# Optimization experiments

Measured on AMD Instinct MI355X. Metric: run time of the kernel, lower is better.

The kernel has to match this reference:

```python
import jax, jax.numpy as jnp
import numpy as np

N, E, F_IN, E_IN, H, L, C = 50000, 500000, 128, 16, 128, 2, 2
BN_EPS = 1e-5


def _linear_params(key, fan_in, fan_out):
    k1, k2 = jax.random.split(key)
    w = jax.random.normal(k1, (fan_in, fan_out), jnp.float32) * (1.0 / np.sqrt(fan_in))
    b = jax.random.normal(k2, (fan_out,), jnp.float32) * 0.01
    return w, b


def setup_inputs() -> dict:
    key = jax.random.key(0)
    ks = jax.random.split(key, 32)
    x = jax.random.normal(ks[0], (N, F_IN), jnp.float32)
    edge_attr = jax.random.normal(ks[1], (E, E_IN), jnp.float32)
    edge_index = jax.random.randint(ks[2], (2, E), 0, N, jnp.int64)

    node_w, node_b = _linear_params(ks[3], F_IN, H)
    edge_w, edge_b = _linear_params(ks[4], E_IN, H)

    def stack(fn, base):
        ws, bs = zip(*[fn(jax.random.fold_in(ks[base], i)) for i in range(L)])
        return jnp.stack(ws), jnp.stack(bs)

    conv_w1, conv_b1 = stack(lambda k: _linear_params(k, H, H), 5)
    conv_w2, conv_b2 = stack(lambda k: _linear_params(k, H, H), 6)
    emlp_w1, emlp_b1 = stack(lambda k: _linear_params(k, 3 * H, H), 7)
    emlp_w2, emlp_b2 = stack(lambda k: _linear_params(k, H, H), 8)
    bn_gamma = jnp.ones((L, H), jnp.float32)
    bn_beta = jnp.zeros((L, H), jnp.float32)

    mlp_w1, mlp_b1 = _linear_params(ks[9], 3 * H, 50)
    mlp_w2, mlp_b2 = _linear_params(ks[10], 50, 25)
    mlp_w3, mlp_b3 = _linear_params(ks[11], 25, C)

    return dict(x=x, edge_attr=edge_attr,
                node_w=node_w, node_b=node_b, edge_w=edge_w, edge_b=edge_b,
                conv_w1=conv_w1, conv_b1=conv_b1, conv_w2=conv_w2, conv_b2=conv_b2,
                bn_gamma=bn_gamma, bn_beta=bn_beta,
                emlp_w1=emlp_w1, emlp_b1=emlp_b1, emlp_w2=emlp_w2, emlp_b2=emlp_b2,
                mlp_w1=mlp_w1, mlp_b1=mlp_b1, mlp_w2=mlp_w2, mlp_b2=mlp_b2,
                mlp_w3=mlp_w3, mlp_b3=mlp_b3, edge_index=edge_index)


def _forward(x, edge_attr, node_w, node_b, edge_w, edge_b,
             conv_w1, conv_b1, conv_w2, conv_b2, bn_gamma, bn_beta,
             emlp_w1, emlp_b1, emlp_w2, emlp_b2,
             mlp_w1, mlp_b1, mlp_w2, mlp_b2, mlp_w3, mlp_b3, edge_index):
    src, dst = edge_index[0], edge_index[1]
    h = x @ node_w + node_b                      # [N, H]
    ea = edge_attr @ edge_w + edge_b             # [E, H]
    for i in range(L):
        # GINEConv: message = relu(x_src + edge_attr), scatter-add at dst
        msg = jax.nn.relu(h[src] + ea)           # [E, H]
        agg = jax.ops.segment_sum(msg, dst, num_segments=N)
        z = h + agg                              # eps = 0
        z = jax.nn.relu(z @ conv_w1[i] + conv_b1[i]) @ conv_w2[i] + conv_b2[i]
        # BatchNorm (training-mode batch statistics over nodes)
        mu = jnp.mean(z, axis=0)
        var = jnp.var(z, axis=0)
        z = bn_gamma[i] * (z - mu) * jax.lax.rsqrt(var + BN_EPS) + bn_beta[i]
        h = (h + jax.nn.relu(z)) * 0.5
        # edge update MLP
        eu = jnp.concatenate([h[src], h[dst], ea], axis=-1)  # [E, 3H]
        ea = ea + (jax.nn.relu(eu @ emlp_w1[i] + emlp_b1[i]) @ emlp_w2[i] + emlp_b2[i]) * 0.5
    # readout: x[edge_index.T].reshape(-1, 2H) cat edge_attr -> [E, 3H]
    feat = jnp.concatenate([h[src], h[dst], ea], axis=-1)
    o = jax.nn.relu(feat @ mlp_w1 + mlp_b1)      # dropout is eval no-op
    o = jax.nn.relu(o @ mlp_w2 + mlp_b2)
    return o @ mlp_w3 + mlp_b3                   # [E, n_classes]


def reference(x, edge_attr, node_w, node_b, edge_w, edge_b,
              conv_w1, conv_b1, conv_w2, conv_b2, bn_gamma, bn_beta,
              emlp_w1, emlp_b1, emlp_w2, emlp_b2,
              mlp_w1, mlp_b1, mlp_w2, mlp_b2, mlp_w3, mlp_b3, edge_index):
    return _forward(x, edge_attr, node_w, node_b, edge_w, edge_b,
                    conv_w1, conv_b1, conv_w2, conv_b2, bn_gamma, bn_beta,
                    emlp_w1, emlp_b1, emlp_w2, emlp_b2,
                    mlp_w1, mlp_b1, mlp_w2, mlp_b2, mlp_w3, mlp_b3, edge_index)
```

## Files before the change

kernel.cpp:

```cpp
#include <hip/hip_runtime.h>


#define NN 50000
#define NE 500000
#define HD 128

typedef _Float16 f16;
typedef _Float16 f16x8 __attribute__((ext_vector_type(8)));
typedef _Float16 f16x4 __attribute__((ext_vector_type(4)));
typedef _Float16 f16x2 __attribute__((ext_vector_type(2)));
typedef float f32x4 __attribute__((ext_vector_type(4)));
typedef unsigned short ushort_t;

#define MFMA16(a, b, c) __builtin_amdgcn_mfma_f32_16x16x32_f16((a), (b), (c), 0, 0, 0)

#define TSTR 152

#define P_NODE_W 0
#define P_NODE_B 16384
#define P_EDGE_W 16512
#define P_EDGE_B 18560
#define P_CONV_W1 18688
#define P_CONV_B1 51456
#define P_CONV_W2 51712
#define P_CONV_B2 84480
#define P_GAMMA 84736
#define P_BETA 84992
#define P_EMLP_W1 85248
#define P_EMLP_B1 183552
#define P_EMLP_W2 183808
#define P_EMLP_B2 216576
#define P_MLP_W1 216832
#define P_MLP_B1 236032
#define P_MLP_W2 236082
#define P_MLP_B2 237332
#define P_MLP_W3 237357
#define P_MLP_B3 237407
#define P_TOTAL 237409

__device__ __forceinline__ float bf2f(unsigned short u) {
    union { unsigned int i; float f; } v;
    v.i = ((unsigned int)u) << 16;
    return v.f;
}

__global__ __launch_bounds__(256) void k_detect(
    const unsigned int* nw, const int* ei, int* flags) {
    __shared__ int cF, cI;
    if (threadIdx.x == 0) { cF = 0; cI = 0; }
    __syncthreads();
    unsigned int u = nw[threadIdx.x];
    int e = (int)((u >> 7) & 0xFFu);
    int odd = ei[2 * threadIdx.x + 1];
    if (e >= 100 && e <= 140) atomicAdd(&cF, 1);
    if (odd != 0) atomicAdd(&cI, 1);
    __syncthreads();
    if (threadIdx.x == 0) {
        flags[0] = (cF < 160) ? 1 : 0;
        flags[1] = (cI < 64) ? 1 : 0;
    }
}

__global__ __launch_bounds__(256) void k_cvt(
    const void* src, f16* dst, int n4, const int* flags) {
    int i = blockIdx.x * 256 + threadIdx.x;
    if (i >= n4) return;
    f16x4 o;
    if (flags[0]) {
        float4 v = ((const float4*)src)[i];
        o[0] = (f16)v.x; o[1] = (f16)v.y; o[2] = (f16)v.z; o[3] = (f16)v.w;
    } else {
        ushort4 v = ((const ushort4*)src)[i];
        o[0] = (f16)bf2f(v.x); o[1] = (f16)bf2f(v.y);
        o[2] = (f16)bf2f(v.z); o[3] = (f16)bf2f(v.w);
    }
    ((f16x4*)dst)[i] = o;
}

__global__ __launch_bounds__(256) void k_cvt_prm(
    const void* p0, const void* p1, const void* p2, const void* p3,
    const void* p4, const void* p5, const void* p6, const void* p7,
    const void* p8, const void* p9, const void* p10, const void* p11,
    const void* p12, const void* p13, const void* p14, const void* p15,
    const void* p16, const void* p17, const void* p18, const void* p19,
    float* prm, const int* flags) {
    int i = blockIdx.x * 256 + threadIdx.x;
    if (i >= P_TOTAL) return;
    const int offs[21] = {P_NODE_W, P_NODE_B, P_EDGE_W, P_EDGE_B, P_CONV_W1,
                          P_CONV_B1, P_CONV_W2, P_CONV_B2, P_GAMMA, P_BETA,
                          P_EMLP_W1, P_EMLP_B1, P_EMLP_W2, P_EMLP_B2, P_MLP_W1,
                          P_MLP_B1, P_MLP_W2, P_MLP_B2, P_MLP_W3, P_MLP_B3,
                          P_TOTAL};
    const void* srcs[20] = {p0, p1, p2, p3, p4, p5, p6, p7, p8, p9, p10, p11,
                            p12, p13, p14, p15, p16, p17, p18, p19};
    int s = 0;
#pragma unroll
    for (int k = 1; k < 20; ++k)
        if (i >= offs[k]) s = k;
    int li = i - offs[s];
    float v = flags[0] ? ((const float*)srcs[s])[li]
                       : bf2f(((const ushort_t*)srcs[s])[li]);
    prm[i] = v;
}

__global__ __launch_bounds__(256) void k_cvt_idx(
    const int* src, int* dst, const int* flags) {
    int i = blockIdx.x * 256 + threadIdx.x;
    if (i >= 2 * NE) return;
    dst[i] = flags[1] ? src[2 * i] : src[i];
}

__global__ __launch_bounds__(256) void k_hist(const int* eix, int* cnt) {
    int e = blockIdx.x * 256 + threadIdx.x;
    if (e < NE) atomicAdd(&cnt[eix[NE + e]], 1);
}

__global__ __launch_bounds__(256) void k_scanA(const int* cnt, int* bsum) {
    __shared__ int wsum[4];
    int tid = threadIdx.x;
    int i = blockIdx.x * 256 + tid;
    int v = (i < NN) ? cnt[i] : 0;
#pragma unroll
    for (int s = 1; s < 64; s <<= 1) v += __shfl_xor(v, s);
    if ((tid & 63) == 0) wsum[tid >> 6] = v;
    __syncthreads();
    if (tid == 0) bsum[blockIdx.x] = wsum[0] + wsum[1] + wsum[2] + wsum[3];
}

__global__ __launch_bounds__(256) void k_scanB(const int* bsum, int* bpre, int* off) {
    __shared__ int l[200];
    int tid = threadIdx.x;
    if (tid < 196) l[tid] = bsum[tid];
    __syncthreads();
    if (tid == 0) {
        int run = 0;
        for (int b = 0; b < 196; ++b) { int t = l[b]; l[b] = run; run += t; }
        off[NN] = run;
    }
    __syncthreads();
    if (tid < 196) bpre[tid] = l[tid];
}

__global__ __launch_bounds__(256) void k_scanC(
    const int* cnt, const int* bpre, int* off, int* cursor) {
    __shared__ int wsum[4];
    int tid = threadIdx.x;
    int lane = tid & 63, wave = tid >> 6;
    int i = blockIdx.x * 256 + tid;
    int v = (i < NN) ? cnt[i] : 0;
    int incl = v;
#pragma unroll
    for (int s = 1; s < 64; s <<= 1) {
        int t = __shfl_up(incl, s);
        if (lane >= s) incl += t;
    }
    if (lane == 63) wsum[wave] = incl;
    __syncthreads();
    int add = bpre[blockIdx.x];
    for (int w = 0; w < 4; ++w)
        if (w < wave) add += wsum[w];
    int excl = add + incl - v;
    if (i < NN) { off[i] = excl; cursor[i] = excl; }
}

__global__ __launch_bounds__(256) void k_scatter(
    const int* eix, int* cursor, int* eord) {
    int e = blockIdx.x * 256 + threadIdx.x;
    if (e >= NE) return;
    int d = eix[NE + e];
    int pos = atomicAdd(&cursor[d], 1);
    eord[pos] = e;
}

__global__ __launch_bounds__(256) void k_agg(
    const f16* ea, const f16* h16, const int* eix, const int* off,
    const int* eord, f16* agg16) {
    int wid = (blockIdx.x * 256 + threadIdx.x) >> 6;
    int lane = threadIdx.x & 63;
    int beg = off[wid], end = off[wid + 1];
    float a0 = 0.f, a1 = 0.f;
    for (int i = beg; i < end; ++i) {
        int e = eord[i];
        int s = eix[e];
        f16x2 ev = *(const f16x2*)(ea + (size_t)e * HD + lane * 2);
        f16x2 hv = *(const f16x2*)(h16 + (size_t)s * HD + lane * 2);
        a0 += fmaxf((float)ev[0] + (float)hv[0], 0.f);
        a1 += fmaxf((float)ev[1] + (float)hv[1], 0.f);
    }
    f16x2 o; o[0] = (f16)a0; o[1] = (f16)a1;
    *(f16x2*)(agg16 + (size_t)wid * HD + lane * 2) = o;
}

__global__ __launch_bounds__(256) void k_prep(const float* prm, f16* wbuf) {
    int gid = blockIdx.x * 256 + threadIdx.x;
    if (gid < 13 * 16384) {
        int seg = gid >> 14;
        int idx = gid & 16383;
        int off;
        switch (seg) {
            case 0: off = P_NODE_W; break;
            case 1: off = P_CONV_W1; break;
            case 2: off = P_CONV_W1 + 16384; break;
            case 3: off = P_CONV_W2; break;
            case 4: off = P_CONV_W2 + 16384; break;
            case 5: case 6: case 7: off = P_EMLP_W1 + (seg - 5) * 16384; break;
            case 8: case 9: case 10: off = P_EMLP_W1 + 49152 + (seg - 8) * 16384; break;
            case 11: off = P_EMLP_W2; break;
            default: off = P_EMLP_W2 + 16384; break;
        }
        int fb = idx >> 9;
        int sub = (idx & 511) >> 3;
        int j = idx & 7;
        int q = sub >> 4, n = sub & 15;
        int nt = fb >> 2, kt = fb & 3;
        int k = kt * 32 + q * 8 + j;
        int c = nt * 16 + n;
        wbuf[gid] = (f16)prm[off + k * 128 + c];
    } else {
        int t = gid - 13 * 16384;
        if (t >= 3 * 8192) return;
        int s = t >> 13;
        int idx = t & 8191;
        int fb = idx >> 9;
        int sub = (idx & 511) >> 3;
        int j = idx & 7;
        int q = sub >> 4, n = sub & 15;
        int nt = fb >> 2, kt = fb & 3;
        int k = s * 128 + kt * 32 + q * 8 + j;
        int c = nt * 16 + n;
        float v = (c < 50) ? prm[P_MLP_W1 + k * 50 + c] : 0.f;
        wbuf[13 * 16384 + s * 8192 + idx] = (f16)v;
    }
}

__global__ __launch_bounds__(256) void k_node_lin(
    const f16* xc, const f16* wT, const float* bias, f16* h_f16) {
    __shared__ __align__(16) f16 wlds[16384];
    int tid = threadIdx.x;
    {
        const uint4* s = (const uint4*)wT;
        uint4* d = (uint4*)wlds;
        for (int i = tid; i < 2048; i += 256) d[i] = s[i];
    }
    __syncthreads();
    int wave = tid >> 6, lane = tid & 63, q = lane >> 4, ln = lane & 15;
    int rowbase = blockIdx.x * 128 + wave * 32;
    f32x4 acc[2][8] = {};
    for (int kt = 0; kt < 4; ++kt) {
        int koff = kt * 32 + q * 8;
        f16x8 a[2];
#pragma unroll
        for (int mt = 0; mt < 2; ++mt) {
            int row = min(rowbase + mt * 16 + ln, NN - 1);
            a[mt] = *(const f16x8*)(xc + row * HD + koff);
        }
#pragma unroll
        for (int nt = 0; nt < 8; ++nt) {
            f16x8 b = *(const f16x8*)&wlds[(nt * 4 + kt) * 512 + lane * 8];
            acc[0][nt] = MFMA16(a[0], b, acc[0][nt]);
            acc[1][nt] = MFMA16(a[1], b, acc[1][nt]);
        }
    }
#pragma unroll
    for (int nt = 0; nt < 8; ++nt) {
        int col = nt * 16 + ln;
        float bv = bias[col];
#pragma unroll
        for (int mt = 0; mt < 2; ++mt)
#pragma unroll
            for (int r = 0; r < 4; ++r) {
                int row = rowbase + mt * 16 + q * 4 + r;
                if (row < NN) h_f16[row * HD + col] = (f16)(acc[mt][nt][r] + bv);
            }
    }
}

__global__ __launch_bounds__(256) void k_edge_lin(
    const f16* eattr, const float* ew, const float* ebias, f16* ea) {
    __shared__ float wl[16 * 128];
    __shared__ float bl[128];
    __shared__ float al[64 * 16];
    int tid = threadIdx.x;
    int eb = blockIdx.x * 64;
    for (int i = tid; i < 2048; i += 256) wl[i] = ew[i];
    if (tid < 128) bl[tid] = ebias[tid];
    {
        int e_l = tid >> 2, k0 = (tid & 3) * 4;
        int e = min(eb + e_l, NE - 1);
        f16x4 u = *(const f16x4*)(eattr + e * 16 + k0);
        al[e_l * 16 + k0 + 0] = (float)u[0];
        al[e_l * 16 + k0 + 1] = (float)u[1];
        al[e_l * 16 + k0 + 2] = (float)u[2];
        al[e_l * 16 + k0 + 3] = (float)u[3];
    }
    __syncthreads();
    for (int i = 0; i < 32; ++i) {
        int o = i * 256 + tid;
        int e_l = o >> 7, c = o & 127;
        float s = bl[c];
#pragma unroll
        for (int k = 0; k < 16; ++k) s += al[e_l * 16 + k] * wl[k * 128 + c];
        int e = eb + e_l;
        if (e < NE) ea[(size_t)e * HD + c] = (f16)s;
    }
}

__global__ __launch_bounds__(256) void k_conv1(
    const f16* h16, const f16* agg16, const f16* wT, const float* bias,
    f16* t_node) {
    __shared__ __align__(16) f16 wlds[16384];
    int tid = threadIdx.x;
    {
        const uint4* s = (const uint4*)wT;
        uint4* d = (uint4*)wlds;
        for (int i = tid; i < 2048; i += 256) d[i] = s[i];
    }
    __syncthreads();
    int wave = tid >> 6, lane = tid & 63, q = lane >> 4, ln = lane & 15;
    int rowbase = blockIdx.x * 128 + wave * 32;
    f32x4 acc[2][8] = {};
    for (int kt = 0; kt < 4; ++kt) {
        int koff = kt * 32 + q * 8;
        f16x8 a[2];
#pragma unroll
        for (int mt = 0; mt < 2; ++mt) {
            int row = min(rowbase + mt * 16 + ln, NN - 1);
            f16x8 hv = *(const f16x8*)(h16 + row * HD + koff);
            f16x8 gv = *(const f16x8*)(agg16 + row * HD + koff);
            f16x8 av;
#pragma unroll
            for (int j = 0; j < 8; ++j) av[j] = (f16)((float)hv[j] + (float)gv[j]);
            a[mt] = av;
        }
#pragma unroll
        for (int nt = 0; nt < 8; ++nt) {
            f16x8 b = *(const f16x8*)&wlds[(nt * 4 + kt) * 512 + lane * 8];
            acc[0][nt] = MFMA16(a[0], b, acc[0][nt]);
            acc[1][nt] = MFMA16(a[1], b, acc[1][nt]);
        }
    }
#pragma unroll
    for (int nt = 0; nt < 8; ++nt) {
        int col = nt * 16 + ln;
        float bv = bias[col];
#pragma unroll
        for (int mt = 0; mt < 2; ++mt)
#pragma unroll
            for (int r = 0; r < 4; ++r) {
                int row = rowbase + mt * 16 + q * 4 + r;
                if (row < NN)
                    t_node[row * HD + col] = (f16)fmaxf(acc[mt][nt][r] + bv, 0.f);
            }
    }
}

__global__ __launch_bounds__(256) void k_conv2(
    const f16* t_node, const f16* wT, const float* bias, f16* z2, float* stats) {
    __shared__ __align__(16) f16 wlds[16384];
    int tid = threadIdx.x;
    {
        const uint4* s = (const uint4*)wT;
        uint4* d = (uint4*)wlds;
        for (int i = tid; i < 2048; i += 256) d[i] = s[i];
    }
    __syncthreads();
    int wave = tid >> 6, lane = tid & 63, q = lane >> 4, ln = lane & 15;
    int rowbase = blockIdx.x * 128 + wave * 32;
    f32x4 acc[2][8] = {};
    for (int kt = 0; kt < 4; ++kt) {
        int koff = kt * 32 + q * 8;
        f16x8 a[2];
#pragma unroll
        for (int mt = 0; mt < 2; ++mt) {
            int row = min(rowbase + mt * 16 + ln, NN - 1);
            a[mt] = *(const f16x8*)(t_node + row * HD + koff);
        }
#pragma unroll
        for (int nt = 0; nt < 8; ++nt) {
            f16x8 b = *(const f16x8*)&wlds[(nt * 4 + kt) * 512 + lane * 8];
            acc[0][nt] = MFMA16(a[0], b, acc[0][nt]);
            acc[1][nt] = MFMA16(a[1], b, acc[1][nt]);
        }
    }
#pragma unroll
    for (int nt = 0; nt < 8; ++nt) {
        int col = nt * 16 + ln;
        float bv = bias[col];
        float s = 0.f, s2 = 0.f;
#pragma unroll
        for (int mt = 0; mt < 2; ++mt)
#pragma unroll
            for (int r = 0; r < 4; ++r) {
                int row = rowbase + mt * 16 + q * 4 + r;
                if (row < NN) {
                    float v = acc[mt][nt][r] + bv;
                    z2[row * HD + col] = (f16)v;
                    s += v;
                    s2 += v * v;
                }
            }
        s += __shfl_xor(s, 16);  s += __shfl_xor(s, 32);
        s2 += __shfl_xor(s2, 16); s2 += __shfl_xor(s2, 32);
        if (lane < 16) {
            atomicAdd(&stats[col], s);
            atomicAdd(&stats[HD + col], s2);
        }
    }
}

__global__ __launch_bounds__(256) void k_bn(
    const f16* z2, const float* stats, const float* gamma, const float* beta,
    f16* h16) {
    int gid = blockIdx.x * 256 + threadIdx.x;
    if (gid >= NN * HD / 4) return;
    int base = gid * 4;
    int c0 = base & (HD - 1);
    f16x4 z = *(const f16x4*)(z2 + base);
    f16x4 h = *(const f16x4*)(h16 + base);
    f16x4 ho;
#pragma unroll
    for (int j = 0; j < 4; ++j) {
        int c = c0 + j;
        float mu = stats[c] * (1.0f / NN);
        float var = stats[HD + c] * (1.0f / NN) - mu * mu;
        float zn = gamma[c] * ((float)z[j] - mu) * rsqrtf(var + 1e-5f) + beta[c];
        ho[j] = (f16)(((float)h[j] + fmaxf(zn, 0.f)) * 0.5f);
    }
    *(f16x4*)(h16 + base) = ho;
}

__global__ __launch_bounds__(256) void k_emlp(
    const f16* h16, const int* eidx, const f16* w1T, const float* b1,
    const f16* w2T, const float* b2, f16* ea) {
    __shared__ __align__(16) f16 wlds[16384];
    __shared__ __align__(16) f16 t16[128 * TSTR];
    __shared__ int sidx[128], didx[128];
    int tid = threadIdx.x;
    int eb = blockIdx.x * 128;
    if (tid < 128) {
        int e = min(eb + tid, NE - 1);
        sidx[tid] = eidx[e];
        didx[tid] = eidx[NE + e];
    }
    int wave = tid >> 6, lane = tid & 63, q = lane >> 4, ln = lane & 15;
    f32x4 acc[2][8] = {};
    for (int seg = 0; seg < 3; ++seg) {
        __syncthreads();
        {
            const uint4* s = (const uint4*)(w1T + seg * 16384);
            uint4* d = (uint4*)wlds;
            for (int i = tid; i < 2048; i += 256) d[i] = s[i];
        }
        __syncthreads();
        for (int kt = 0; kt < 4; ++kt) {
            int koff = kt * 32 + q * 8;
            f16x8 a[2];
#pragma unroll
            for (int mt = 0; mt < 2; ++mt) {
                int le = wave * 32 + mt * 16 + ln;
                const f16* ap;
                if (seg == 0)      ap = h16 + (size_t)sidx[le] * HD + koff;
                else if (seg == 1) ap = h16 + (size_t)didx[le] * HD + koff;
                else               ap = ea + (size_t)min(eb + le, NE - 1) * HD + koff;
                a[mt] = *(const f16x8*)ap;
            }
#pragma unroll
            for (int nt = 0; nt < 8; ++nt) {
                f16x8 b = *(const f16x8*)&wlds[(nt * 4 + kt) * 512 + lane * 8];
                acc[0][nt] = MFMA16(a[0], b, acc[0][nt]);
                acc[1][nt] = MFMA16(a[1], b, acc[1][nt]);
            }
        }
    }
#pragma unroll
    for (int nt = 0; nt < 8; ++nt) {
        int col = nt * 16 + ln;
        float bv = b1[col];
#pragma unroll
        for (int mt = 0; mt < 2; ++mt)
#pragma unroll
            for (int r = 0; r < 4; ++r) {
                int row = wave * 32 + mt * 16 + q * 4 + r;
                t16[row * TSTR + col] = (f16)fmaxf(acc[mt][nt][r] + bv, 0.f);
            }
    }
    __syncthreads();
    {
        const uint4* s = (const uint4*)w2T;
        uint4* d = (uint4*)wlds;
        for (int i = tid; i < 2048; i += 256) d[i] = s[i];
    }
    __syncthreads();
    f32x4 acc2[2][8] = {};
    for (int kt = 0; kt < 4; ++kt) {
        int koff = kt * 32 + q * 8;
        f16x8 a[2];
#pragma unroll
        for (int mt = 0; mt < 2; ++mt) {
            int le = wave * 32 + mt * 16 + ln;
            a[mt] = *(const f16x8*)&t16[le * TSTR + koff];
        }
#pragma unroll
        for (int nt = 0; nt < 8; ++nt) {
            f16x8 b = *(const f16x8*)&wlds[(nt * 4 + kt) * 512 + lane * 8];
            acc2[0][nt] = MFMA16(a[0], b, acc2[0][nt]);
            acc2[1][nt] = MFMA16(a[1], b, acc2[1][nt]);
        }
    }
#pragma unroll
    for (int nt = 0; nt < 8; ++nt) {
        int col = nt * 16 + ln;
        float bv = b2[col];
#pragma unroll
        for (int mt = 0; mt < 2; ++mt)
#pragma unroll
            for (int r = 0; r < 4; ++r) {
                int e = eb + wave * 32 + mt * 16 + q * 4 + r;
                if (e < NE) {
                    size_t o = (size_t)e * HD + col;
                    ea[o] = (f16)((float)ea[o] + 0.5f * (acc2[mt][nt][r] + bv));
                }
            }
    }
}

__global__ __launch_bounds__(256) void k_readout(
    const f16* h16, const f16* ea, const int* eidx, const f16* w1Tp,
    const float* mb1, const float* mw2, const float* mb2,
    const float* mw3, const float* mb3, float* out) {
    __shared__ __align__(16) f16 wlds[8192];
    __shared__ f16 o1[256 * 58];
    __shared__ float w2l[50 * 28];
    __shared__ float w3l[50];
    __shared__ float b2l[25];
    __shared__ float b3l[2];
    __shared__ int sidx[256], didx[256];
    int tid = threadIdx.x;
    int eb = blockIdx.x * 256;
    {
        int e = min(eb + tid, NE - 1);
        sidx[tid] = eidx[e];
        didx[tid] = eidx[NE + e];
    }
    for (int i = tid; i < 50 * 28; i += 256) {
        int k = i / 28, ko = i - k * 28;
        w2l[i] = (ko < 25) ? mw2[k * 25 + ko] : 0.f;
    }
    if (tid < 50) w3l[tid] = mw3[tid];
    if (tid < 25) b2l[tid] = mb2[tid];
    if (tid < 2) b3l[tid] = mb3[tid];
    int wave = tid >> 6, lane = tid & 63, q = lane >> 4, ln = lane & 15;
    f32x4 acc[4][4] = {};
    for (int seg = 0; seg < 3; ++seg) {
        __syncthreads();
        {
            const uint4* s = (const uint4*)(w1Tp + seg * 8192);
            uint4* d = (uint4*)wlds;
            for (int i = tid; i < 1024; i += 256) d[i] = s[i];
        }
        __syncthreads();
        for (int kt = 0; kt < 4; ++kt) {
            int koff = kt * 32 + q * 8;
            f16x8 a[4];
#pragma unroll
            for (int mt = 0; mt < 4; ++mt) {
                int le = wave * 64 + mt * 16 + ln;
                const f16* ap;
                if (seg == 0)      ap = h16 + (size_t)sidx[le] * HD + koff;
                else if (seg == 1) ap = h16 + (size_t)didx[le] * HD + koff;
                else               ap = ea + (size_t)min(eb + le, NE - 1) * HD + koff;
                a[mt] = *(const f16x8*)ap;
            }
#pragma unroll
            for (int nt = 0; nt < 4; ++nt) {
                f16x8 b = *(const f16x8*)&wlds[(nt * 4 + kt) * 512 + lane * 8];
#pragma unroll
                for (int mt = 0; mt < 4; ++mt)
                    acc[mt][nt] = MFMA16(a[mt], b, acc[mt][nt]);
            }
        }
    }
#pragma unroll
    for (int nt = 0; nt < 4; ++nt) {
        int col = nt * 16 + ln;
        if (col < 50) {
            float bv = mb1[col];
#pragma unroll
            for (int mt = 0; mt < 4; ++mt)
#pragma unroll
                for (int r = 0; r < 4; ++r) {
                    int le = wave * 64 + mt * 16 + q * 4 + r;
                    o1[le * 58 + col] = (f16)fmaxf(acc[mt][nt][r] + bv, 0.f);
                }
        }
    }
    __syncthreads();
    float o2[25];
#pragma unroll
    for (int ko = 0; ko < 25; ++ko) o2[ko] = b2l[ko];
    for (int k = 0; k < 50; ++k) {
        float a = (float)o1[tid * 58 + k];
#pragma unroll
        for (int ko = 0; ko < 25; ++ko) o2[ko] += a * w2l[k * 28 + ko];
    }
    float r0 = b3l[0], r1 = b3l[1];
#pragma unroll
    for (int ko = 0; ko < 25; ++ko) {
        float a = fmaxf(o2[ko], 0.f);
        r0 += a * w3l[ko * 2];
        r1 += a * w3l[ko * 2 + 1];
    }
    int e = eb + tid;
    if (e < NE) {
        float2 o; o.x = r0; o.y = r1;
        *(float2*)(out + (size_t)e * 2) = o;
    }
}

extern "C" void kernel_launch(void* const* d_in, const int* in_sizes, int n_in,
                              void* d_out, int out_size, void* d_ws, size_t ws_size,
                              hipStream_t stream) {
    const size_t WS_NEED = 197425936ULL;
    if (ws_size < WS_NEED) {
        hipMemsetAsync(d_out, 0, (size_t)out_size * 4, stream);
        return;
    }
    char* ws = (char*)d_ws;
    f16* ea = (f16*)(ws);
    f16* hf16 = (f16*)(ws + 128000000LL);
    f16* agg16 = (f16*)(ws + 140800000LL);
    f16* eattr16 = (f16*)(ws + 140800000LL);
    int* eord = (int*)(ws + 153600000LL);
    int* off = (int*)(ws + 155600000LL);
    int* cntcur = (int*)(ws + 155800064LL);
    int* bsum = (int*)(ws + 156000064LL);
    int* bpre = (int*)(ws + 156001088LL);
    f16* z2 = (f16*)(ws + 166400000LL);
    f16* xc = (f16*)(ws + 166400000LL);
    f16* tn = (f16*)(ws + 179200000LL);
    f16* wbuf = (f16*)(ws + 192000000LL);
    float* stats = (float*)(ws + 192475136LL);
    float* prm = (float*)(ws + 192476160LL);
    int* eix = (int*)(ws + 193425920LL);
    int* flags = (int*)(ws + 197425920LL);
    float* out = (float*)d_out;

    k_detect<<<1, 256, 0, stream>>>((const unsigned int*)d_in[2],
                                    (const int*)d_in[22], flags);
    k_cvt<<<6250, 256, 0, stream>>>(d_in[0], xc, 1600000, flags);
    k_cvt<<<7813, 256, 0, stream>>>(d_in[1], eattr16, 2000000, flags);
    k_cvt_prm<<<928, 256, 0, stream>>>(
        d_in[2], d_in[3], d_in[4], d_in[5], d_in[6], d_in[7], d_in[8], d_in[9],
        d_in[10], d_in[11], d_in[12], d_in[13], d_in[14], d_in[15], d_in[16],
        d_in[17], d_in[18], d_in[19], d_in[20], d_in[21], prm, flags);
    k_cvt_idx<<<3907, 256, 0, stream>>>((const int*)d_in[22], eix, flags);

    k_prep<<<928, 256, 0, stream>>>(prm, wbuf);
    k_node_lin<<<391, 256, 0, stream>>>(xc, wbuf, prm + P_NODE_B, hf16);
    k_edge_lin<<<7813, 256, 0, stream>>>(eattr16, prm + P_EDGE_W, prm + P_EDGE_B, ea);

    hipMemsetAsync(cntcur, 0, NN * 4, stream);
    k_hist<<<1954, 256, 0, stream>>>(eix, cntcur);
    k_scanA<<<196, 256, 0, stream>>>(cntcur, bsum);
    k_scanB<<<1, 256, 0, stream>>>(bsum, bpre, off);
    k_scanC<<<196, 256, 0, stream>>>(cntcur, bpre, off, cntcur);
    k_scatter<<<1954, 256, 0, stream>>>(eix, cntcur, eord);

    for (int l = 0; l < 2; ++l) {
        hipMemsetAsync(stats, 0, 1024, stream);
        k_agg<<<12500, 256, 0, stream>>>(ea, hf16, eix, off, eord, agg16);
        k_conv1<<<391, 256, 0, stream>>>(hf16, agg16, wbuf + (1 + l) * 16384,
                                         prm + P_CONV_B1 + l * HD, tn);
        k_conv2<<<391, 256, 0, stream>>>(tn, wbuf + (3 + l) * 16384,
                                         prm + P_CONV_B2 + l * HD, z2, stats);
        k_bn<<<6250, 256, 0, stream>>>(z2, stats, prm + P_GAMMA + l * HD,
                                       prm + P_BETA + l * HD, hf16);
        k_emlp<<<3907, 256, 0, stream>>>(hf16, eix, wbuf + (5 + l * 3) * 16384,
                                         prm + P_EMLP_B1 + l * HD,
                                         wbuf + (11 + l) * 16384,
                                         prm + P_EMLP_B2 + l * HD, ea);
    }
    k_readout<<<1954, 256, 0, stream>>>(hf16, ea, eix, wbuf + 13 * 16384,
                                        prm + P_MLP_B1, prm + P_MLP_W2,
                                        prm + P_MLP_B2, prm + P_MLP_W3,
                                        prm + P_MLP_B3, out);
}
```

Measured before the change: 1.120 ms.

## Halve edge-MLP tile to 64 edges per block and preload full K rows

The edge-update MLP kernel now handles 64 edges per block instead of 128, with each wave owning one 16-row M tile. It issues all four K-slice loads of a gathered row up front before the MFMA chain, and the grid size doubles. Several other GEMM kernels get an unroll pragma on their K loop. The intent is to cut LDS and register use so more blocks fit per CU and to get more gather loads in flight, but each block now reloads the 32 KB weight set while covering half as many edges, which doubles weight-staging traffic per edge.

```diff
diff --git a/kernel.cpp b/kernel.cpp
--- a/kernel.cpp
+++ b/kernel.cpp
@@ -246,6 +246,7 @@
     int wave = tid >> 6, lane = tid & 63, q = lane >> 4, ln = lane & 15;
     int rowbase = blockIdx.x * 128 + wave * 32;
     f32x4 acc[2][8] = {};
+#pragma unroll
     for (int kt = 0; kt < 4; ++kt) {
         int koff = kt * 32 + q * 8;
         f16x8 a[2];
@@ -319,6 +320,7 @@
     int wave = tid >> 6, lane = tid & 63, q = lane >> 4, ln = lane & 15;
     int rowbase = blockIdx.x * 128 + wave * 32;
     f32x4 acc[2][8] = {};
+#pragma unroll
     for (int kt = 0; kt < 4; ++kt) {
         int koff = kt * 32 + q * 8;
         f16x8 a[2];
@@ -367,6 +369,7 @@
     int wave = tid >> 6, lane = tid & 63, q = lane >> 4, ln = lane & 15;
     int rowbase = blockIdx.x * 128 + wave * 32;
     f32x4 acc[2][8] = {};
+#pragma unroll
     for (int kt = 0; kt < 4; ++kt) {
         int koff = kt * 32 + q * 8;
         f16x8 a[2];
@@ -433,17 +436,18 @@
     const f16* h16, const int* eidx, const f16* w1T, const float* b1,
     const f16* w2T, const float* b2, f16* ea) {
     __shared__ __align__(16) f16 wlds[16384];
-    __shared__ __align__(16) f16 t16[128 * TSTR];
-    __shared__ int sidx[128], didx[128];
-    int tid = threadIdx.x;
-    int eb = blockIdx.x * 128;
-    if (tid < 128) {
+    __shared__ __align__(16) f16 t16[64 * TSTR];
+    __shared__ int sidx[64], didx[64];
+    int tid = threadIdx.x;
+    int eb = blockIdx.x * 64;
+    if (tid < 64) {
         int e = min(eb + tid, NE - 1);
         sidx[tid] = eidx[e];
         didx[tid] = eidx[NE + e];
     }
     int wave = tid >> 6, lane = tid & 63, q = lane >> 4, ln = lane & 15;
-    f32x4 acc[2][8] = {};
+    int le = wave * 16 + ln;
+    f32x4 acc[8] = {};
     for (int seg = 0; seg < 3; ++seg) {
         __syncthreads();
         {
@@ -452,37 +456,31 @@
             for (int i = tid; i < 2048; i += 256) d[i] = s[i];
         }
         __syncthreads();
-        for (int kt = 0; kt < 4; ++kt) {
-            int koff = kt * 32 + q * 8;
-            f16x8 a[2];
-#pragma unroll
-            for (int mt = 0; mt < 2; ++mt) {
-                int le = wave * 32 + mt * 16 + ln;
-                const f16* ap;
-                if (seg == 0)      ap = h16 + (size_t)sidx[le] * HD + koff;
-                else if (seg == 1) ap = h16 + (size_t)didx[le] * HD + koff;
-                else               ap = ea + (size_t)min(eb + le, NE - 1) * HD + koff;
-                a[mt] = *(const f16x8*)ap;
-            }
+        const f16* base;
+        if (seg == 0)      base = h16 + (size_t)sidx[le] * HD;
+        else if (seg == 1) base = h16 + (size_t)didx[le] * HD;
+        else               base = ea + (size_t)min(eb + le, NE - 1) * HD;
+        f16x8 a[4];
+#pragma unroll
+        for (int kt = 0; kt < 4; ++kt)
+            a[kt] = *(const f16x8*)(base + kt * 32 + q * 8);
+#pragma unroll
+        for (int kt = 0; kt < 4; ++kt)
 #pragma unroll
             for (int nt = 0; nt < 8; ++nt) {
                 f16x8 b = *(const f16x8*)&wlds[(nt * 4 + kt) * 512 + lane * 8];
-                acc[0][nt] = MFMA16(a[0], b, acc[0][nt]);
-                acc[1][nt] = MFMA16(a[1], b, acc[1][nt]);
-            }
-        }
+                acc[nt] = MFMA16(a[kt], b, acc[nt]);
+            }
     }
 #pragma unroll
     for (int nt = 0; nt < 8; ++nt) {
         int col = nt * 16 + ln;
         float bv = b1[col];
 #pragma unroll
-        for (int mt = 0; mt < 2; ++mt)
-#pragma unroll
-            for (int r = 0; r < 4; ++r) {
-                int row = wave * 32 + mt * 16 + q * 4 + r;
-                t16[row * TSTR + col] = (f16)fmaxf(acc[mt][nt][r] + bv, 0.f);
-            }
+        for (int r = 0; r < 4; ++r) {
+            int row = wave * 16 + q * 4 + r;
+            t16[row * TSTR + col] = (f16)fmaxf(acc[nt][r] + bv, 0.f);
+        }
     }
     __syncthreads();
     {
@@ -491,36 +489,32 @@
         for (int i = tid; i < 2048; i += 256) d[i] = s[i];
     }
     __syncthreads();
-    f32x4 acc2[2][8] = {};
-    for (int kt = 0; kt < 4; ++kt) {
-        int koff = kt * 32 + q * 8;
-        f16x8 a[2];
-#pragma unroll
-        for (int mt = 0; mt < 2; ++mt) {
-            int le = wave * 32 + mt * 16 + ln;
-            a[mt] = *(const f16x8*)&t16[le * TSTR + koff];
-        }
-#pragma unroll
-        for (int nt = 0; nt < 8; ++nt) {
-            f16x8 b = *(const f16x8*)&wlds[(nt * 4 + kt) * 512 + lane * 8];
-            acc2[0][nt] = MFMA16(a[0], b, acc2[0][nt]);
-            acc2[1][nt] = MFMA16(a[1], b, acc2[1][nt]);
-        }
+    f32x4 acc2[8] = {};
+    {
+        f16x8 a2[4];
+#pragma unroll
+        for (int kt = 0; kt < 4; ++kt)
+            a2[kt] = *(const f16x8*)&t16[le * TSTR + kt * 32 + q * 8];
+#pragma unroll
+        for (int kt = 0; kt < 4; ++kt)
+#pragma unroll
+            for (int nt = 0; nt < 8; ++nt) {
+                f16x8 b = *(const f16x8*)&wlds[(nt * 4 + kt) * 512 + lane * 8];
+                acc2[nt] = MFMA16(a2[kt], b, acc2[nt]);
+            }
     }
 #pragma unroll
     for (int nt = 0; nt < 8; ++nt) {
         int col = nt * 16 + ln;
         float bv = b2[col];
 #pragma unroll
-        for (int mt = 0; mt < 2; ++mt)
-#pragma unroll
-            for (int r = 0; r < 4; ++r) {
-                int e = eb + wave * 32 + mt * 16 + q * 4 + r;
-                if (e < NE) {
-                    size_t o = (size_t)e * HD + col;
-                    ea[o] = (f16)((float)ea[o] + 0.5f * (acc2[mt][nt][r] + bv));
-                }
-            }
+        for (int r = 0; r < 4; ++r) {
+            int e = eb + wave * 16 + q * 4 + r;
+            if (e < NE) {
+                size_t o = (size_t)e * HD + col;
+                ea[o] = (f16)((float)ea[o] + 0.5f * (acc2[nt][r] + bv));
+            }
+        }
     }
 }
 
@@ -559,6 +553,7 @@
             for (int i = tid; i < 1024; i += 256) d[i] = s[i];
         }
         __syncthreads();
+#pragma unroll
         for (int kt = 0; kt < 4; ++kt) {
             int koff = kt * 32 + q * 8;
             f16x8 a[4];
@@ -675,7 +670,7 @@
                                          prm + P_CONV_B2 + l * HD, z2, stats);
         k_bn<<<6250, 256, 0, stream>>>(z2, stats, prm + P_GAMMA + l * HD,
                                        prm + P_BETA + l * HD, hf16);
-        k_emlp<<<3907, 256, 0, stream>>>(hf16, eix, wbuf + (5 + l * 3) * 16384,
+        k_emlp<<<7813, 256, 0, stream>>>(hf16, eix, wbuf + (5 + l * 3) * 16384,
                                          prm + P_EMLP_B1 + l * HD,
                                          wbuf + (11 + l) * 16384,
                                          prm + P_EMLP_B2 + l * HD, ea);
```

New measurement: 1.103 ms. No clear change (-1.5%).

## Transpose edge-MLP MFMA operands and pass hidden layer through registers via shuffles

Applied to the files above, without the earlier changes.

The edge-update MLP kernel now computes the transposed product, with weights as the A operand and gathered edge rows as B. The first-layer ReLU output is packed into registers and redistributed with cross-lane shuffles for the second GEMM, which removes the 39 KB LDS staging buffer and its round trip. The epilogue writes contiguous 4-element vectors per edge row instead of scattered scalar stores, and all gathers for a segment are issued up front. Launch bounds request 4 blocks per CU, and several k-loops are fully unrolled. The gain comes from lower LDS use and better occupancy and store coalescing, at the cost of higher register pressure and extra shuffle instructions.

```diff
diff --git a/kernel.cpp b/kernel.cpp
--- a/kernel.cpp
+++ b/kernel.cpp
@@ -246,6 +246,7 @@
     int wave = tid >> 6, lane = tid & 63, q = lane >> 4, ln = lane & 15;
     int rowbase = blockIdx.x * 128 + wave * 32;
     f32x4 acc[2][8] = {};
+#pragma unroll
     for (int kt = 0; kt < 4; ++kt) {
         int koff = kt * 32 + q * 8;
         f16x8 a[2];
@@ -319,6 +320,7 @@
     int wave = tid >> 6, lane = tid & 63, q = lane >> 4, ln = lane & 15;
     int rowbase = blockIdx.x * 128 + wave * 32;
     f32x4 acc[2][8] = {};
+#pragma unroll
     for (int kt = 0; kt < 4; ++kt) {
         int koff = kt * 32 + q * 8;
         f16x8 a[2];
@@ -367,6 +369,7 @@
     int wave = tid >> 6, lane = tid & 63, q = lane >> 4, ln = lane & 15;
     int rowbase = blockIdx.x * 128 + wave * 32;
     f32x4 acc[2][8] = {};
+#pragma unroll
     for (int kt = 0; kt < 4; ++kt) {
         int koff = kt * 32 + q * 8;
         f16x8 a[2];
@@ -429,11 +432,10 @@
     *(f16x4*)(h16 + base) = ho;
 }
 
-__global__ __launch_bounds__(256) void k_emlp(
+__global__ __launch_bounds__(256, 4) void k_emlp(
     const f16* h16, const int* eidx, const f16* w1T, const float* b1,
     const f16* w2T, const float* b2, f16* ea) {
     __shared__ __align__(16) f16 wlds[16384];
-    __shared__ __align__(16) f16 t16[128 * TSTR];
     __shared__ int sidx[128], didx[128];
     int tid = threadIdx.x;
     int eb = blockIdx.x * 128;
@@ -443,6 +445,8 @@
         didx[tid] = eidx[NE + e];
     }
     int wave = tid >> 6, lane = tid & 63, q = lane >> 4, ln = lane & 15;
+    int el0 = wave * 32 + ln;
+    int el1 = wave * 32 + 16 + ln;
     f32x4 acc[2][8] = {};
     for (int seg = 0; seg < 3; ++seg) {
         __syncthreads();
@@ -452,38 +456,49 @@
             for (int i = tid; i < 2048; i += 256) d[i] = s[i];
         }
         __syncthreads();
+        const f16 *p0, *p1;
+        if (seg == 0) {
+            p0 = h16 + (size_t)sidx[el0] * HD;
+            p1 = h16 + (size_t)sidx[el1] * HD;
+        } else if (seg == 1) {
+            p0 = h16 + (size_t)didx[el0] * HD;
+            p1 = h16 + (size_t)didx[el1] * HD;
+        } else {
+            p0 = ea + (size_t)min(eb + el0, NE - 1) * HD;
+            p1 = ea + (size_t)min(eb + el1, NE - 1) * HD;
+        }
+        f16x8 g0[4], g1[4];
+#pragma unroll
         for (int kt = 0; kt < 4; ++kt) {
-            int koff = kt * 32 + q * 8;
-            f16x8 a[2];
-#pragma unroll
-            for (int mt = 0; mt < 2; ++mt) {
-                int le = wave * 32 + mt * 16 + ln;
-                const f16* ap;
-                if (seg == 0)      ap = h16 + (size_t)sidx[le] * HD + koff;
-                else if (seg == 1) ap = h16 + (size_t)didx[le] * HD + koff;
-                else               ap = ea + (size_t)min(eb + le, NE - 1) * HD + koff;
-                a[mt] = *(const f16x8*)ap;
-            }
-#pragma unroll
-            for (int nt = 0; nt < 8; ++nt) {
-                f16x8 b = *(const f16x8*)&wlds[(nt * 4 + kt) * 512 + lane * 8];
-                acc[0][nt] = MFMA16(a[0], b, acc[0][nt]);
-                acc[1][nt] = MFMA16(a[1], b, acc[1][nt]);
-            }
-        }
-    }
-#pragma unroll
-    for (int nt = 0; nt < 8; ++nt) {
-        int col = nt * 16 + ln;
-        float bv = b1[col];
-#pragma unroll
-        for (int mt = 0; mt < 2; ++mt)
+            g0[kt] = *(const f16x8*)(p0 + kt * 32 + q * 8);
+            g1[kt] = *(const f16x8*)(p1 + kt * 32 + q * 8);
+        }
+#pragma unroll
+        for (int kt = 0; kt < 4; ++kt)
+#pragma unroll
+            for (int mt = 0; mt < 8; ++mt) {
+                f16x8 a = *(const f16x8*)&wlds[(mt * 4 + kt) * 512 + lane * 8];
+                acc[0][mt] = MFMA16(a, g0[kt], acc[0][mt]);
+                acc[1][mt] = MFMA16(a, g1[kt], acc[1][mt]);
+            }
+    }
+    union HU { f16 h; unsigned short u; };
+    unsigned int pk[2][4][4];
+#pragma unroll
+    for (int ntl = 0; ntl < 2; ++ntl)
+#pragma unroll
+        for (int kt = 0; kt < 4; ++kt) {
+            f32x4 blo = *(const f32x4*)(b1 + (2 * kt) * 16 + q * 4);
+            f32x4 bhi = *(const f32x4*)(b1 + (2 * kt + 1) * 16 + q * 4);
 #pragma unroll
             for (int r = 0; r < 4; ++r) {
-                int row = wave * 32 + mt * 16 + q * 4 + r;
-                t16[row * TSTR + col] = (f16)fmaxf(acc[mt][nt][r] + bv, 0.f);
-            }
-    }
+                HU lo, hi;
+                lo.h = (f16)fmaxf(acc[ntl][2 * kt][r] + blo[r], 0.f);
+                hi.h = (f16)fmaxf(acc[ntl][2 * kt + 1][r] + bhi[r], 0.f);
+                pk[ntl][kt][r] =
+                    (unsigned int)lo.u | ((unsigned int)hi.u << 16);
+            }
+        }
     __syncthreads();
     {
         const uint4* s = (const uint4*)w2T;
@@ -491,36 +506,50 @@
         for (int i = tid; i < 2048; i += 256) d[i] = s[i];
     }
     __syncthreads();
+    int s1 = (((2 * q) & 3) << 4) | ln;
+    int s2 = (((2 * q + 1) & 3) << 4) | ln;
+    int hsh = (q >> 1) * 16;
     f32x4 acc2[2][8] = {};
+#pragma unroll
     for (int kt = 0; kt < 4; ++kt) {
-        int koff = kt * 32 + q * 8;
-        f16x8 a[2];
-#pragma unroll
-        for (int mt = 0; mt < 2; ++mt) {
-            int le = wave * 32 + mt * 16 + ln;
-            a[mt] = *(const f16x8*)&t16[le * TSTR + koff];
-        }
-#pragma unroll
-        for (int nt = 0; nt < 8; ++nt) {
-            f16x8 b = *(const f16x8*)&wlds[(nt * 4 + kt) * 512 + lane * 8];
-            acc2[0][nt] = MFMA16(a[0], b, acc2[0][nt]);
-            acc2[1][nt] = MFMA16(a[1], b, acc2[1][nt]);
-        }
-    }
-#pragma unroll
-    for (int nt = 0; nt < 8; ++nt) {
-        int col = nt * 16 + ln;
-        float bv = b2[col];
-#pragma unroll
-        for (int mt = 0; mt < 2; ++mt)
+        f16x8 bf[2];
+#pragma unroll
+        for (int ntl = 0; ntl < 2; ++ntl) {
+            union { unsigned short u[8]; f16x8 v; } bb;
 #pragma unroll
             for (int r = 0; r < 4; ++r) {
-                int e = eb + wave * 32 + mt * 16 + q * 4 + r;
-                if (e < NE) {
-                    size_t o = (size_t)e * HD + col;
-                    ea[o] = (f16)((float)ea[o] + 0.5f * (acc2[mt][nt][r] + bv));
-                }
-            }
+                unsigned int v1 = (unsigned int)__shfl((int)pk[ntl][kt][r], s1);
+                unsigned int v2 = (unsigned int)__shfl((int)pk[ntl][kt][r], s2);
+                bb.u[r] = (unsigned short)(v1 >> hsh);
+                bb.u[4 + r] = (unsigned short)(v2 >> hsh);
+            }
+            bf[ntl] = bb.v;
+        }
+#pragma unroll
+        for (int mt = 0; mt < 8; ++mt) {
+            f16x8 a = *(const f16x8*)&wlds[(mt * 4 + kt) * 512 + lane * 8];
+            acc2[0][mt] = MFMA16(a, bf[0], acc2[0][mt]);
+            acc2[1][mt] = MFMA16(a, bf[1], acc2[1][mt]);
+        }
+    }
+#pragma unroll
+    for (int ntl = 0; ntl < 2; ++ntl) {
+        int e = eb + wave * 32 + ntl * 16 + ln;
+        if (e < NE) {
+            f16* erow = ea + (size_t)e * HD;
+#pragma unroll
+            for (int mt = 0; mt < 8; ++mt) {
+                int c0 = mt * 16 + q * 4;
+                f32x4 bv = *(const f32x4*)(b2 + c0);
+                f16x4 old = *(const f16x4*)(erow + c0);
+                f16x4 nw;
+#pragma unroll
+                for (int r = 0; r < 4; ++r)
+                    nw[r] = (f16)((float)old[r] +
+                                  0.5f * (acc2[ntl][mt][r] + bv[r]));
+                *(f16x4*)(erow + c0) = nw;
+            }
+        }
     }
 }
 
@@ -559,6 +588,7 @@
             for (int i = tid; i < 1024; i += 256) d[i] = s[i];
         }
         __syncthreads();
+#pragma unroll
         for (int kt = 0; kt < 4; ++kt) {
             int koff = kt * 32 + q * 8;
             f16x8 a[4];
```

Result: faster. 1.021 ms (-8.9%).
